# Optimization experiments

Hardware: AMD Instinct MI355X
Metric: run time of the kernel (lower is better)

## Reference

```python
import jax, jax.numpy as jnp
import numpy as np

TOKEN_DIM = 768
HIDDEN_DIM = 384
PATCH_SCALE = 2
SELECTED_RATIO = 0.15


def setup_inputs() -> dict:
    key = jax.random.key(0)
    ks = jax.random.split(key, 12)
    B, T, D = 32, 1024, TOKEN_DIM
    Thr = T * PATCH_SCALE * PATCH_SCALE  # 4096
    flat_dim = D * PATCH_SCALE * PATCH_SCALE  # 3072
    H = HIDDEN_DIM
    s = lambda fan_in: 1.0 / np.sqrt(fan_in)
    inp = {
        "base_tokens": jax.random.normal(ks[0], (B, T, D), jnp.float32),
        "highres_tokens": jax.random.normal(ks[1], (B, Thr, D), jnp.float32),
        "selection_scores": jax.random.normal(ks[2], (B, T), jnp.float32),
        # local_refine: Linear(flat_dim,H) -> GELU -> Linear(H,D)
        "W1": jax.random.uniform(ks[3], (flat_dim, H), jnp.float32, -s(flat_dim), s(flat_dim)),
        "b1": jax.random.uniform(ks[4], (H,), jnp.float32, -s(flat_dim), s(flat_dim)),
        "W2": jax.random.uniform(ks[5], (H, D), jnp.float32, -s(H), s(H)),
        "b2": jax.random.uniform(ks[6], (D,), jnp.float32, -s(H), s(H)),
        # blend_gate: Linear(2D+1,H) -> SiLU -> Linear(H,1)
        "Wg1": jax.random.uniform(ks[7], (2 * D + 1, H), jnp.float32, -s(2 * D + 1), s(2 * D + 1)),
        "bg1": jax.random.uniform(ks[8], (H,), jnp.float32, -s(2 * D + 1), s(2 * D + 1)),
        "Wg2": jax.random.uniform(ks[9], (H, 1), jnp.float32, -s(H), s(H)),
        "bg2": jax.random.uniform(ks[10], (1,), jnp.float32, -s(H), s(H)),
    }
    return inp


def reference(base_tokens, highres_tokens, selection_scores,
              W1, b1, W2, b2, Wg1, bg1, Wg2, bg2):
    B, T, D = base_tokens.shape
    S = PATCH_SCALE
    g = int(round(np.sqrt(T)))  # coarse grid side
    # strided patch reshape: [B, g, S, g, S, D] -> [B, g, g, S, S, D] -> [B, T, S*S*D]
    local = highres_tokens.reshape(B, g, S, g, S, D)
    local = local.transpose(0, 1, 3, 2, 4, 5).reshape(B, T, S * S * D)
    # local refine MLP (exact-erf GELU matches torch nn.GELU default)
    h = jax.nn.gelu(jnp.einsum('btf,fh->bth', local, W1) + b1, approximate=False)
    refined_local = jnp.einsum('bth,hd->btd', h, W2) + b2
    # blend gate
    gate_in = jnp.concatenate([base_tokens, refined_local, selection_scores[..., None]], axis=-1)
    hg = jax.nn.silu(jnp.einsum('btf,fh->bth', gate_in, Wg1) + bg1)
    gate = jax.nn.sigmoid(jnp.einsum('bth,ho->bto', hg, Wg2) + bg2)  # [B, T, 1]
    # top-k selection mask (static k)
    topk = max(1, int(round(T * SELECTED_RATIO)))
    topk_idx = jax.lax.top_k(selection_scores, topk)[1]  # [B, k]
    mask = jnp.zeros((B, T), base_tokens.dtype).at[jnp.arange(B)[:, None], topk_idx].set(1.0)
    refined = base_tokens + mask[..., None] * gate * (refined_local - base_tokens)
    return refined
```

## Files before the change

### kernel.cpp

```cpp
#include <hip/hip_runtime.h>
#include <cstdint>

#define NB    32
#define NTOK  1024
#define D_    768
#define NHR   4096
#define HID   384
#define KSEL  154
#define MSEL  4928
#define MT_   77
#define FLAT  3072

typedef short  s16x8 __attribute__((ext_vector_type(8)));
typedef unsigned short u16x8 __attribute__((ext_vector_type(8)));
typedef unsigned short u16x4 __attribute__((ext_vector_type(4)));
typedef float  f32x4 __attribute__((ext_vector_type(4)));

__device__ inline unsigned short f2bf(float f) {
    uint32_t u = __builtin_bit_cast(uint32_t, f);
    u += 0x7FFFu + ((u >> 16) & 1u);
    return (unsigned short)(u >> 16);
}
__device__ inline float bf2f(unsigned short h) {
    uint32_t u = ((uint32_t)h) << 16;
    return __builtin_bit_cast(float, u);
}

#define OFF_SEL   0
#define OFF_RMAP  32768
#define OFF_GPART 163840
#define OFF_W1T   401408
#define OFF_W2T   2760704
#define OFF_WG1T  3350528
#define OFF_ABASE 4530176
#define OFF_H     12099584
#define OFF_RL    15884288
#define DOUT_P0   32505856
#define DOUT_P1   (DOUT_P0 + MSEL * HID * 4)

__global__ __launch_bounds__(1024) void prep_kernel(
    const float* __restrict__ scores, int* __restrict__ sel, int* __restrict__ rmap,
    const float* __restrict__ W1, const float* __restrict__ W2, const float* __restrict__ Wg1,
    unsigned short* __restrict__ W1t, unsigned short* __restrict__ W2t,
    unsigned short* __restrict__ Wg1t)
{
    __shared__ float s[NTOK];
    __shared__ int cnt;
    __shared__ unsigned short T[4][64][66];
    const int bid = blockIdx.x;
    if (bid < NB) {
        const int b = bid;
        const int t = threadIdx.x;
        s[t] = scores[b * NTOK + t];
        if (t == 0) cnt = 0;
        __syncthreads();
        float v = s[t];
        int rank = 0;
        for (int j = 0; j < NTOK; ++j) {
            float vj = s[j];
            rank += (vj > v) || (vj == v && j < t);
        }
        int rm = -1;
        if (rank < KSEL) {
            int pos = atomicAdd(&cnt, 1);
            rm = b * KSEL + pos;
            sel[rm] = t;
        }
        rmap[b * NTOK + t] = rm;
    } else {
        const int g = threadIdx.x >> 8;
        const int tid = threadIdx.x & 255;
        const int tile = (bid - NB) * 4 + g;
        const float* src; unsigned short* dst; int K, N, kt, nt;
        if (tile < 288)      { src = W1;  dst = W1t;  K = FLAT; N = HID; nt = tile % 6;  kt = tile / 6;  }
        else if (tile < 360) { int l = tile - 288; src = W2;  dst = W2t;  K = HID;  N = D_;  nt = l % 12; kt = l / 12; }
        else                 { int l = tile - 360; src = Wg1; dst = Wg1t; K = 1536; N = HID; nt = l % 6;  kt = l / 6;  }
        const int k0 = kt * 64, n0 = nt * 64;
        {
            const int ln = tid & 63, kc = tid >> 6;
            #pragma unroll
            for (int j = 0; j < 16; ++j)
                T[g][ln][kc * 16 + j] = f2bf(src[(uint64_t)(k0 + kc * 16 + j) * N + n0 + ln]);
        }
        __syncthreads();
        {
            const int row = tid >> 2, c0 = (tid & 3) * 16;
            u16x8 v0, v1;
            #pragma unroll
            for (int p = 0; p < 8; ++p) { v0[p] = T[g][row][c0 + p]; v1[p] = T[g][row][c0 + 8 + p]; }
            *(u16x8*)(dst + (uint64_t)(n0 + row) * K + k0 + c0) = v0;
            *(u16x8*)(dst + (uint64_t)(n0 + row) * K + k0 + c0 + 8) = v1;
        }
    }
}

__global__ __launch_bounds__(256) void gather_kernel(
    const int* __restrict__ sel, const float* __restrict__ highres,
    const float* __restrict__ base,
    unsigned short* __restrict__ Aloc, unsigned short* __restrict__ Abase) {
    const int r = blockIdx.x;
    const int b = r / KSEL;
    const int t = sel[r];
    const int gy = t >> 5, gx = t & 31;
    for (int ch = threadIdx.x; ch < 480; ch += 256) {
        if (ch < 384) {
            int k8 = ch * 8;
            int p = k8 / D_;
            int col = k8 - p * D_;
            int hr = (gy * 2 + (p >> 1)) * 64 + gx * 2 + (p & 1);
            const float4* s4 = (const float4*)(highres + ((uint64_t)b * NHR + hr) * D_ + col);
            float4 v0 = s4[0], v1 = s4[1];
            u16x8 v;
            v[0]=f2bf(v0.x); v[1]=f2bf(v0.y); v[2]=f2bf(v0.z); v[3]=f2bf(v0.w);
            v[4]=f2bf(v1.x); v[5]=f2bf(v1.y); v[6]=f2bf(v1.z); v[7]=f2bf(v1.w);
            *(u16x8*)(Aloc + (uint64_t)r * FLAT + k8) = v;
        } else {
            int col = (ch - 384) * 8;
            const float4* s4 = (const float4*)(base + ((uint64_t)b * NTOK + t) * D_ + col);
            float4 v0 = s4[0], v1 = s4[1];
            u16x8 v;
            v[0]=f2bf(v0.x); v[1]=f2bf(v0.y); v[2]=f2bf(v0.z); v[3]=f2bf(v0.w);
            v[4]=f2bf(v1.x); v[5]=f2bf(v1.y); v[6]=f2bf(v1.z); v[7]=f2bf(v1.w);
            *(u16x8*)(Abase + (uint64_t)r * D_ + col) = v;
        }
    }
}

template <int MODE>
__global__ __launch_bounds__(256) void gemm_mfma(
    const unsigned short* __restrict__ A0,
    const unsigned short* __restrict__ A1,
    const unsigned short* __restrict__ Bt,
    const float* __restrict__ bias,
    const int* __restrict__ sel,
    const float* __restrict__ scores,
    const float* __restrict__ WgLast,
    const float* __restrict__ Wg2,
    void* __restrict__ Cout,
    float* __restrict__ Pout,
    float* __restrict__ gpart)
{
    constexpr int K = MODE == 0 ? FLAT : (MODE == 1 ? HID : 2 * D_);
    constexpr int N = MODE == 1 ? D_ : HID;
    constexpr int NT = N / 64;
    constexpr int KLEN = (MODE == 0) ? 1536 : K;
    constexpr int NSTEP = KLEN / 64;

    const int lin = blockIdx.x;
    const int xcd = lin & 7;
    int j = lin >> 3;
    const int ntile = j % NT; j /= NT;
    const int mhi = j % 10;
    const int split = j / 10;
    const int mt = mhi * 8 + xcd;
    if (mt >= MT_) return;
    const int m0 = mt * 64;
    const int n0 = ntile * 64;
    const int kb = split * 1536;
    float* P = (MODE == 0) ? (Pout + (uint64_t)split * MSEL * HID) : nullptr;

    __shared__ unsigned short As[2][64 * 64];
    __shared__ unsigned short Bs[2][64 * 64];
    __shared__ float scv[64];

    const int tid = threadIdx.x;
    const int lane = tid & 63;
    const int wid = tid >> 6;
    const int wm = wid >> 1;
    const int wn = wid & 1;

    if (MODE == 2 && tid < 64) {
        int r = m0 + tid, b = r / KSEL, t = sel[r];
        scv[tid] = scores[b * NTOK + t];
    }

    const int sr0 = tid >> 3;
    const int sc0 = tid & 7;

    auto loadA = [&](int k0, int half, s16x8& dst) {
        int r = sr0 + half * 32;
        int k = k0 + sc0 * 8;
        const unsigned short* p;
        if (MODE == 2) {
            p = (k < D_) ? (A0 + (uint64_t)(m0 + r) * D_ + k)
                         : (A1 + (uint64_t)(m0 + r) * D_ + (k - D_));
        } else {
            p = A0 + (uint64_t)(m0 + r) * K + k;
        }
        dst = *(const s16x8*)p;
    };
    auto loadB = [&](int k0, int half, s16x8& dst) {
        int r = sr0 + half * 32;
        dst = *(const s16x8*)(Bt + (uint64_t)(n0 + r) * K + k0 + sc0 * 8);
    };
    auto writeTile = [&](int buf, s16x8* a, s16x8* b) {
        #pragma unroll
        for (int half = 0; half < 2; ++half) {
            int r = sr0 + half * 32;
            int c = sc0 ^ (r & 7);
            *(s16x8*)&As[buf][r * 64 + c * 8] = a[half];
            *(s16x8*)&Bs[buf][r * 64 + c * 8] = b[half];
        }
    };

    f32x4 acc[2][2];
    #pragma unroll
    for (int i = 0; i < 2; ++i)
        #pragma unroll
        for (int jj = 0; jj < 2; ++jj) acc[i][jj] = (f32x4){0.f, 0.f, 0.f, 0.f};

    s16x8 aR[2], bR[2];
    loadA(kb, 0, aR[0]); loadA(kb, 1, aR[1]);
    loadB(kb, 0, bR[0]); loadB(kb, 1, bR[1]);
    writeTile(0, aR, bR);
    __syncthreads();
    if (NSTEP > 1) {
        loadA(kb + 64, 0, aR[0]); loadA(kb + 64, 1, aR[1]);
        loadB(kb + 64, 0, bR[0]); loadB(kb + 64, 1, bR[1]);
    }

    int cur = 0;
    for (int t = 0; t < NSTEP; ++t) {
        #pragma unroll
        for (int kk = 0; kk < 2; ++kk) {
            s16x8 af[2], bfr[2];
            #pragma unroll
            for (int i = 0; i < 2; ++i) {
                int row  = wm * 32 + i * 16 + (lane & 15);
                int cch  = (kk * 4 + (lane >> 4)) ^ (row & 7);
                af[i] = *(const s16x8*)&As[cur][row * 64 + cch * 8];
                int nrow = wn * 32 + i * 16 + (lane & 15);
                int cchb = (kk * 4 + (lane >> 4)) ^ (nrow & 7);
                bfr[i] = *(const s16x8*)&Bs[cur][nrow * 64 + cchb * 8];
            }
            #pragma unroll
            for (int i = 0; i < 2; ++i)
                #pragma unroll
                for (int jj = 0; jj < 2; ++jj)
                    acc[i][jj] = __builtin_amdgcn_mfma_f32_16x16x32_bf16(af[i], bfr[jj], acc[i][jj], 0, 0, 0);
        }
        if (t + 1 < NSTEP) {
            writeTile(cur ^ 1, aR, bR);
            __syncthreads();
            if (t + 2 < NSTEP) {
                int k0 = kb + (t + 2) * 64;
                loadA(k0, 0, aR[0]); loadA(k0, 1, aR[1]);
                loadB(k0, 0, bR[0]); loadB(k0, 1, bR[1]);
            }
            cur ^= 1;
        }
    }

    if (MODE == 2) {
        float wg2v[2] = { Wg2[n0 + wn * 32 + (lane & 15)],
                          Wg2[n0 + wn * 32 + 16 + (lane & 15)] };
        float psum[2][4];
        #pragma unroll
        for (int i = 0; i < 2; ++i)
            #pragma unroll
            for (int reg = 0; reg < 4; ++reg) psum[i][reg] = 0.f;
        #pragma unroll
        for (int i = 0; i < 2; ++i) {
            #pragma unroll
            for (int jj = 0; jj < 2; ++jj) {
                #pragma unroll
                for (int reg = 0; reg < 4; ++reg) {
                    int m = m0 + wm * 32 + i * 16 + (lane >> 4) * 4 + reg;
                    int n = n0 + wn * 32 + jj * 16 + (lane & 15);
                    float x = acc[i][jj][reg] + bias[n] + scv[m - m0] * WgLast[n];
                    x = x / (1.0f + __expf(-x));
                    psum[i][reg] += x * wg2v[jj];
                }
            }
        }
        #pragma unroll
        for (int mask = 1; mask < 16; mask <<= 1)
            #pragma unroll
            for (int i = 0; i < 2; ++i)
                #pragma unroll
                for (int reg = 0; reg < 4; ++reg)
                    psum[i][reg] += __shfl_xor(psum[i][reg], mask);
        if ((lane & 15) == 0) {
            #pragma unroll
            for (int i = 0; i < 2; ++i)
                #pragma unroll
                for (int reg = 0; reg < 4; ++reg) {
                    int m = m0 + wm * 32 + i * 16 + (lane >> 4) * 4 + reg;
                    gpart[m * 12 + ntile * 2 + wn] = psum[i][reg];
                }
        }
        return;
    }
    #pragma unroll
    for (int i = 0; i < 2; ++i) {
        #pragma unroll
        for (int jj = 0; jj < 2; ++jj) {
            #pragma unroll
            for (int reg = 0; reg < 4; ++reg) {
                int m = m0 + wm * 32 + i * 16 + (lane >> 4) * 4 + reg;
                int n = n0 + wn * 32 + jj * 16 + (lane & 15);
                if (MODE == 0) {
                    P[(uint64_t)m * HID + n] = acc[i][jj][reg];
                } else {
                    float x = acc[i][jj][reg] + bias[n];
                    ((unsigned short*)Cout)[(uint64_t)m * D_ + n] = f2bf(x);
                }
            }
        }
    }
}

__global__ __launch_bounds__(256) void combine_kernel(
    const float* __restrict__ P0, const float* __restrict__ P1,
    const float* __restrict__ b1, unsigned short* __restrict__ h)
{
    const int idx = (blockIdx.x * 256 + threadIdx.x) * 8;
    const int col = idx % HID;
    float4 a0 = *(const float4*)(P0 + idx), a1 = *(const float4*)(P0 + idx + 4);
    float4 c0 = *(const float4*)(P1 + idx), c1 = *(const float4*)(P1 + idx + 4);
    float4 bb0 = *(const float4*)(b1 + col), bb1 = *(const float4*)(b1 + col + 4);
    float xs[8] = { a0.x + c0.x + bb0.x, a0.y + c0.y + bb0.y,
                    a0.z + c0.z + bb0.z, a0.w + c0.w + bb0.w,
                    a1.x + c1.x + bb1.x, a1.y + c1.y + bb1.y,
                    a1.z + c1.z + bb1.z, a1.w + c1.w + bb1.w };
    u16x8 v;
    #pragma unroll
    for (int p = 0; p < 8; ++p) {
        float x = xs[p];
        x = 0.5f * x * (1.0f + erff(x * 0.70710678118654752f));
        v[p] = f2bf(x);
    }
    *(u16x8*)(h + idx) = v;
}

__global__ __launch_bounds__(256) void finalize_kernel(
    const int* __restrict__ rmap,
    const float* __restrict__ gpart, const float* __restrict__ bg2,
    const float* __restrict__ base, const unsigned short* __restrict__ rl,
    float* __restrict__ out)
{
    const int lane = threadIdx.x & 63;
    const int row = blockIdx.x * 4 + (threadIdx.x >> 6);
    const int rm = rmap[row];

    const uint64_t bo = (uint64_t)row * D_;
    const float4* b4 = (const float4*)(base + bo);
    float4* o4 = (float4*)(out + bo);

    if (rm < 0) {
        #pragma unroll
        for (int i = 0; i < 3; ++i) o4[lane + 64 * i] = b4[lane + 64 * i];
        return;
    }
    const float4* gp = (const float4*)(gpart + (uint64_t)rm * 12);
    float4 g0 = gp[0], g1 = gp[1], g2 = gp[2];
    float sum = g0.x + g0.y + g0.z + g0.w + g1.x + g1.y + g1.z + g1.w
              + g2.x + g2.y + g2.z + g2.w + bg2[0];
    float gate = 1.0f / (1.0f + __expf(-sum));

    const u16x4* r4 = (const u16x4*)(rl + (uint64_t)rm * D_);
    #pragma unroll
    for (int i = 0; i < 3; ++i) {
        int idx = lane + 64 * i;
        float4 bb = b4[idx];
        u16x4 rr = r4[idx];
        float4 oo;
        oo.x = bb.x + gate * (bf2f(rr[0]) - bb.x);
        oo.y = bb.y + gate * (bf2f(rr[1]) - bb.y);
        oo.z = bb.z + gate * (bf2f(rr[2]) - bb.z);
        oo.w = bb.w + gate * (bf2f(rr[3]) - bb.w);
        o4[idx] = oo;
    }
}

extern "C" void kernel_launch(void* const* d_in, const int* in_sizes, int n_in,
                              void* d_out, int out_size, void* d_ws, size_t ws_size,
                              hipStream_t stream) {
    const float* base   = (const float*)d_in[0];
    const float* hires  = (const float*)d_in[1];
    const float* scores = (const float*)d_in[2];
    const float* W1  = (const float*)d_in[3];
    const float* b1  = (const float*)d_in[4];
    const float* W2  = (const float*)d_in[5];
    const float* b2  = (const float*)d_in[6];
    const float* Wg1 = (const float*)d_in[7];
    const float* bg1 = (const float*)d_in[8];
    const float* Wg2 = (const float*)d_in[9];
    const float* bg2 = (const float*)d_in[10];
    float* out = (float*)d_out;

    char* ws = (char*)d_ws;
    int*            sel   = (int*)(ws + OFF_SEL);
    int*            rmap  = (int*)(ws + OFF_RMAP);
    float*          gpart = (float*)(ws + OFF_GPART);
    unsigned short* W1t   = (unsigned short*)(ws + OFF_W1T);
    unsigned short* W2t   = (unsigned short*)(ws + OFF_W2T);
    unsigned short* Wg1t  = (unsigned short*)(ws + OFF_WG1T);
    unsigned short* Abase = (unsigned short*)(ws + OFF_ABASE);
    unsigned short* h     = (unsigned short*)(ws + OFF_H);
    unsigned short* rl    = (unsigned short*)(ws + OFF_RL);
    unsigned short* Aloc  = (unsigned short*)d_out;
    float*          P0    = (float*)((char*)d_out + DOUT_P0);
    float*          P1    = (float*)((char*)d_out + DOUT_P1);

    prep_kernel<<<dim3(NB + 126), dim3(1024), 0, stream>>>(scores, sel, rmap,
                                                           W1, W2, Wg1, W1t, W2t, Wg1t);
    gather_kernel<<<dim3(MSEL), dim3(256), 0, stream>>>(sel, hires, base, Aloc, Abase);
    gemm_mfma<0><<<dim3(8 * 10 * 6 * 2), dim3(256), 0, stream>>>(
        Aloc, nullptr, W1t, nullptr, nullptr, nullptr, nullptr, nullptr, nullptr, P0, nullptr);
    combine_kernel<<<dim3(924), dim3(256), 0, stream>>>(P0, P1, b1, h);
    gemm_mfma<1><<<dim3(8 * 10 * 12), dim3(256), 0, stream>>>(
        h, nullptr, W2t, b2, nullptr, nullptr, nullptr, nullptr, rl, nullptr, nullptr);
    gemm_mfma<2><<<dim3(8 * 10 * 6), dim3(256), 0, stream>>>(
        Abase, rl, Wg1t, bg1, sel, scores, Wg1 + (uint64_t)1536 * HID, Wg2,
        nullptr, nullptr, gpart);
    finalize_kernel<<<dim3(NB * NTOK / 4), dim3(256), 0, stream>>>(rmap, gpart, bg2, base, rl, out);
}
```

Before: 149.4 us.

## Fuse token gather and bf16 conversion into GEMM A-tile loads

Removes the separate gather kernel that copied the selected high-res patches and base tokens into bf16 staging buffers. The first and third GEMMs now read fp32 rows straight from the inputs through per-tile row offset tables in shared memory and convert to bf16 while loading. This saves one launch and a write-then-read round trip of the staging buffers. In exchange, each N-tile block now reads and converts fp32 rows itself, so global reads double in bytes and are repeated across tiles, and the workspace layout is reshuffled.

```diff
diff --git a/kernel.cpp b/kernel.cpp
--- a/kernel.cpp
+++ b/kernel.cpp
@@ -25,6 +25,13 @@
     uint32_t u = ((uint32_t)h) << 16;
     return __builtin_bit_cast(float, u);
 }
+__device__ inline s16x8 cvt8(const float* __restrict__ p) {
+    float4 v0 = *(const float4*)p, v1 = *(const float4*)(p + 4);
+    s16x8 r;
+    r[0]=(short)f2bf(v0.x); r[1]=(short)f2bf(v0.y); r[2]=(short)f2bf(v0.z); r[3]=(short)f2bf(v0.w);
+    r[4]=(short)f2bf(v1.x); r[5]=(short)f2bf(v1.y); r[6]=(short)f2bf(v1.z); r[7]=(short)f2bf(v1.w);
+    return r;
+}
 
 #define OFF_SEL   0
 #define OFF_RMAP  32768
@@ -32,11 +39,10 @@
 #define OFF_W1T   401408
 #define OFF_W2T   2760704
 #define OFF_WG1T  3350528
-#define OFF_ABASE 4530176
-#define OFF_H     12099584
-#define OFF_RL    15884288
-#define DOUT_P0   32505856
-#define DOUT_P1   (DOUT_P0 + MSEL * HID * 4)
+#define OFF_H     4530176
+#define OFF_RL    8314880
+#define DOUT_P0   0
+#define DOUT_P1   (MSEL * HID * 4)
 
 __global__ __launch_bounds__(1024) void prep_kernel(
     const float* __restrict__ scores, int* __restrict__ sel, int* __restrict__ rmap,
@@ -94,42 +100,10 @@
     }
 }
 
-__global__ __launch_bounds__(256) void gather_kernel(
-    const int* __restrict__ sel, const float* __restrict__ highres,
-    const float* __restrict__ base,
-    unsigned short* __restrict__ Aloc, unsigned short* __restrict__ Abase) {
-    const int r = blockIdx.x;
-    const int b = r / KSEL;
-    const int t = sel[r];
-    const int gy = t >> 5, gx = t & 31;
-    for (int ch = threadIdx.x; ch < 480; ch += 256) {
-        if (ch < 384) {
-            int k8 = ch * 8;
-            int p = k8 / D_;
-            int col = k8 - p * D_;
-            int hr = (gy * 2 + (p >> 1)) * 64 + gx * 2 + (p & 1);
-            const float4* s4 = (const float4*)(highres + ((uint64_t)b * NHR + hr) * D_ + col);
-            float4 v0 = s4[0], v1 = s4[1];
-            u16x8 v;
-            v[0]=f2bf(v0.x); v[1]=f2bf(v0.y); v[2]=f2bf(v0.z); v[3]=f2bf(v0.w);
-            v[4]=f2bf(v1.x); v[5]=f2bf(v1.y); v[6]=f2bf(v1.z); v[7]=f2bf(v1.w);
-            *(u16x8*)(Aloc + (uint64_t)r * FLAT + k8) = v;
-        } else {
-            int col = (ch - 384) * 8;
-            const float4* s4 = (const float4*)(base + ((uint64_t)b * NTOK + t) * D_ + col);
-            float4 v0 = s4[0], v1 = s4[1];
-            u16x8 v;
-            v[0]=f2bf(v0.x); v[1]=f2bf(v0.y); v[2]=f2bf(v0.z); v[3]=f2bf(v0.w);
-            v[4]=f2bf(v1.x); v[5]=f2bf(v1.y); v[6]=f2bf(v1.z); v[7]=f2bf(v1.w);
-            *(u16x8*)(Abase + (uint64_t)r * D_ + col) = v;
-        }
-    }
-}
-
 template <int MODE>
 __global__ __launch_bounds__(256) void gemm_mfma(
-    const unsigned short* __restrict__ A0,
-    const unsigned short* __restrict__ A1,
+    const float* __restrict__ Araw,
+    const unsigned short* __restrict__ Abf,
     const unsigned short* __restrict__ Bt,
     const float* __restrict__ bias,
     const int* __restrict__ sel,
@@ -161,6 +135,7 @@
 
     __shared__ unsigned short As[2][64 * 64];
     __shared__ unsigned short Bs[2][64 * 64];
+    __shared__ uint32_t offT[64 * 4];
     __shared__ float scv[64];
 
     const int tid = threadIdx.x;
@@ -169,10 +144,23 @@
     const int wm = wid >> 1;
     const int wn = wid & 1;
 
-    if (MODE == 2 && tid < 64) {
-        int r = m0 + tid, b = r / KSEL, t = sel[r];
-        scv[tid] = scores[b * NTOK + t];
-    }
+    if (tid < 64) {
+        int r = m0 + tid;
+        if (MODE == 0) {
+            int b = r / KSEL, t = sel[r];
+            int gy = t >> 5, gx = t & 31;
+            #pragma unroll
+            for (int p = 0; p < 4; ++p) {
+                int hr = (gy * 2 + (p >> 1)) * 64 + gx * 2 + (p & 1);
+                offT[tid * 4 + p] = (uint32_t)(b * NHR + hr) * D_;
+            }
+        } else if (MODE == 2) {
+            int b = r / KSEL, t = sel[r];
+            offT[tid * 4] = (uint32_t)(b * NTOK + t) * D_;
+            scv[tid] = scores[b * NTOK + t];
+        }
+    }
+    if (MODE != 1) __syncthreads();
 
     const int sr0 = tid >> 3;
     const int sc0 = tid & 7;
@@ -180,14 +168,16 @@
     auto loadA = [&](int k0, int half, s16x8& dst) {
         int r = sr0 + half * 32;
         int k = k0 + sc0 * 8;
-        const unsigned short* p;
-        if (MODE == 2) {
-            p = (k < D_) ? (A0 + (uint64_t)(m0 + r) * D_ + k)
-                         : (A1 + (uint64_t)(m0 + r) * D_ + (k - D_));
+        if (MODE == 0) {
+            int p = k / D_;
+            int col = k - p * D_;
+            dst = cvt8(Araw + offT[r * 4 + p] + col);
+        } else if (MODE == 1) {
+            dst = *(const s16x8*)(Abf + (uint64_t)(m0 + r) * HID + k);
         } else {
-            p = A0 + (uint64_t)(m0 + r) * K + k;
-        }
-        dst = *(const s16x8*)p;
+            if (k < D_) dst = cvt8(Araw + offT[r * 4] + k);
+            else        dst = *(const s16x8*)(Abf + (uint64_t)(m0 + r) * D_ + (k - D_));
+        }
     };
     auto loadB = [&](int k0, int half, s16x8& dst) {
         int r = sr0 + half * 32;
@@ -396,23 +386,20 @@
     unsigned short* W1t   = (unsigned short*)(ws + OFF_W1T);
     unsigned short* W2t   = (unsigned short*)(ws + OFF_W2T);
     unsigned short* Wg1t  = (unsigned short*)(ws + OFF_WG1T);
-    unsigned short* Abase = (unsigned short*)(ws + OFF_ABASE);
     unsigned short* h     = (unsigned short*)(ws + OFF_H);
     unsigned short* rl    = (unsigned short*)(ws + OFF_RL);
-    unsigned short* Aloc  = (unsigned short*)d_out;
     float*          P0    = (float*)((char*)d_out + DOUT_P0);
     float*          P1    = (float*)((char*)d_out + DOUT_P1);
 
     prep_kernel<<<dim3(NB + 126), dim3(1024), 0, stream>>>(scores, sel, rmap,
                                                            W1, W2, Wg1, W1t, W2t, Wg1t);
-    gather_kernel<<<dim3(MSEL), dim3(256), 0, stream>>>(sel, hires, base, Aloc, Abase);
     gemm_mfma<0><<<dim3(8 * 10 * 6 * 2), dim3(256), 0, stream>>>(
-        Aloc, nullptr, W1t, nullptr, nullptr, nullptr, nullptr, nullptr, nullptr, P0, nullptr);
+        hires, nullptr, W1t, nullptr, sel, nullptr, nullptr, nullptr, nullptr, P0, nullptr);
     combine_kernel<<<dim3(924), dim3(256), 0, stream>>>(P0, P1, b1, h);
     gemm_mfma<1><<<dim3(8 * 10 * 12), dim3(256), 0, stream>>>(
-        h, nullptr, W2t, b2, nullptr, nullptr, nullptr, nullptr, rl, nullptr, nullptr);
+        nullptr, h, W2t, b2, nullptr, nullptr, nullptr, nullptr, rl, nullptr, nullptr);
     gemm_mfma<2><<<dim3(8 * 10 * 6), dim3(256), 0, stream>>>(
-        Abase, rl, Wg1t, bg1, sel, scores, Wg1 + (uint64_t)1536 * HID, Wg2,
+        base, rl, Wg1t, bg1, sel, scores, Wg1 + (uint64_t)1536 * HID, Wg2,
         nullptr, nullptr, gpart);
     finalize_kernel<<<dim3(NB * NTOK / 4), dim3(256), 0, stream>>>(rmap, gpart, bg2, base, rl, out);
 }
```

After: 157.9 us. +5.6%, slower.
